# Optimization experiments

Measured on AMD Instinct MI355X. Metric: run time of the kernel, lower is better.

## Reference

```python
import jax, jax.numpy as jnp
import numpy as np

ALPHA = 20.0 / 100.0  # dt / tau


def setup_inputs() -> dict:
    key = jax.random.key(0)
    ks = jax.random.split(key, 5)
    T, B, I, N = 1000, 256, 128, 512
    return {
        "x": jax.random.normal(ks[0], (T, B, I), dtype=jnp.float32),
        "h0": jax.random.normal(ks[1], (B, N), dtype=jnp.float32) * 0.3,
        "W_in": jax.random.normal(ks[2], (N, I), dtype=jnp.float32) / np.sqrt(I),
        "b_in": jax.random.normal(ks[3], (N,), dtype=jnp.float32) * 0.01,
        "W_hh": jax.random.normal(ks[4], (N, N), dtype=jnp.float32) / np.sqrt(N),
    }


def reference(x, h0, W_in, b_in, W_hh):
    # Precompute input projection for all steps in one GEMM: [T,B,N]
    xproj = jnp.einsum("tbi,ni->tbn", x, W_in) + b_in

    def step(h, xp_t):
        h_new = jnp.tanh(xp_t + h @ W_hh.T)
        h = h * (1.0 - ALPHA) + h_new * ALPHA
        return h, h

    hidden, output = jax.lax.scan(step, h0, xproj)
    return output, hidden
```

## Files before the change

### kernel.cpp

```cpp
#include <hip/hip_runtime.h>
#include <hip/hip_bf16.h>


typedef __bf16 bf16;
typedef __bf16 bf16x8 __attribute__((ext_vector_type(8)));
typedef float floatx4 __attribute__((ext_vector_type(4)));
typedef unsigned short u16;
typedef u16 u16x4 __attribute__((ext_vector_type(4)));

#define T_STEPS 1000
#define BATCH 256
#define NDIM 512
#define IDIM 128

__global__ void pack_kernel(const float* __restrict__ W_hh,
                            const float* __restrict__ W_in,
                            bf16x8* __restrict__ Whpack,
                            bf16x8* __restrict__ WinHi,
                            bf16x8* __restrict__ WinLo) {
    int e = blockIdx.x * 256 + threadIdx.x;
    if (e < 32768) {
        int g = e >> 10, s = (e >> 6) & 15, lane = e & 63;
        int n = 16 * g + (lane & 15);
        int k = 32 * s + 8 * (lane >> 4);
        const float* src = W_hh + n * 512 + k;
        bf16x8 v;
#pragma unroll
        for (int j = 0; j < 8; j++) v[j] = (bf16)src[j];
        Whpack[e] = v;
    } else {
        int e2 = e - 32768;
        if (e2 < 8192) {
            int g = e2 >> 8, s = (e2 >> 6) & 3, lane = e2 & 63;
            int n = 16 * g + (lane & 15);
            int i = 32 * s + 8 * (lane >> 4);
            const float* src = W_in + n * 128 + i;
            bf16x8 vh, vl;
#pragma unroll
            for (int j = 0; j < 8; j++) {
                float w = src[j];
                bf16 h = (bf16)w;
                vh[j] = h;
                vl[j] = (bf16)(w - (float)h);
            }
            WinHi[e2] = vh;
            WinLo[e2] = vl;
        }
    }
}

__global__ __launch_bounds__(256)
void xproj_kernel(const float* __restrict__ x,
                  const float* __restrict__ b_in,
                  const bf16x8* __restrict__ WinHi,
                  const bf16x8* __restrict__ WinLo,
                  float* __restrict__ out) {
    int wave = threadIdx.x >> 6, lane = threadIdx.x & 63;
    int m = lane & 15, q = lane >> 4;
    long Mtile = (long)blockIdx.x * 4 + wave;
    long r0 = Mtile * 16;

    bf16x8 ah[4], al[4];
    const float* xrow = x + (r0 + m) * IDIM + q * 8;
#pragma unroll
    for (int s = 0; s < 4; s++) {
#pragma unroll
        for (int j = 0; j < 8; j++) {
            float w = xrow[s * 32 + j];
            bf16 h = (bf16)w;
            ah[s][j] = h;
            al[s][j] = (bf16)(w - (float)h);
        }
    }
    float* orow = out + r0 * NDIM;
#pragma unroll 1
    for (int g = 0; g < 32; g++) {
        floatx4 acc = {0.f, 0.f, 0.f, 0.f};
#pragma unroll
        for (int s = 0; s < 4; s++) {
            bf16x8 bh = WinHi[(g * 4 + s) * 64 + lane];
            bf16x8 bl = WinLo[(g * 4 + s) * 64 + lane];
            acc = __builtin_amdgcn_mfma_f32_16x16x32_bf16(ah[s], bh, acc, 0, 0, 0);
            acc = __builtin_amdgcn_mfma_f32_16x16x32_bf16(al[s], bh, acc, 0, 0, 0);
            acc = __builtin_amdgcn_mfma_f32_16x16x32_bf16(ah[s], bl, acc, 0, 0, 0);
        }
        float b = b_in[16 * g + m];
#pragma unroll
        for (int r = 0; r < 4; r++) {
            orow[(long)(q * 4 + r) * NDIM + 16 * g + m] = acc[r] + b;
        }
    }
}

__global__ __launch_bounds__(512, 2)
void scan_kernel(const float* __restrict__ h0,
                 const bf16x8* __restrict__ Whpack,
                 float* __restrict__ out) {
    extern __shared__ char smem[];
    bf16x8* Wlds = (bf16x8*)smem;
    bf16x8* pack = (bf16x8*)(smem + 128 * 1024);

    const int tid = threadIdx.x;
    const int wave = tid >> 6, lane = tid & 63;
    const int m = lane & 15, q = lane >> 4;
    const int b0 = blockIdx.x * 16;

    bf16x8 Wr[3][16];
    {
        const bf16x8* base = Whpack + (4 * wave) * 1024 + lane;
#pragma unroll
        for (int i = 0; i < 3; i++)
#pragma unroll
            for (int s = 0; s < 16; s++)
                Wr[i][s] = base[(i * 16 + s) * 64];
    }
    for (int r = 0; r < 16; r++) {
        int e = r * 512 + tid;
        int slot = e >> 10;
        int rem = e & 1023;
        Wlds[e] = Whpack[(4 * slot + 3) * 1024 + rem];
    }
    floatx4 h32[4];
#pragma unroll
    for (int i = 0; i < 4; i++) {
        int n0 = (4 * wave + i) * 16 + q * 4;
        h32[i] = *(const floatx4*)(h0 + (b0 + m) * NDIM + n0);
    }
    for (int e = tid; e < 1024; e += 512) {
        int s = e >> 6, l = e & 63;
        const float* src = h0 + (b0 + (l & 15)) * NDIM + s * 32 + 8 * (l >> 4);
        bf16x8 v;
#pragma unroll
        for (int j = 0; j < 8; j++) v[j] = (bf16)src[j];
        pack[e] = v;
    }
    __syncthreads();

    const int wslot = wave * 1024;

#pragma unroll 1
    for (int t = 0; t < T_STEPS; t++) {
        float* row = out + ((long)(t * BATCH + b0 + m)) * NDIM;
        floatx4 xp[4];
#pragma unroll
        for (int i = 0; i < 4; i++) {
            int n0 = (4 * wave + i) * 16 + q * 4;
            xp[i] = *(const floatx4*)(row + n0);
        }

        floatx4 acc[4];
#pragma unroll
        for (int i = 0; i < 4; i++) acc[i] = (floatx4){0.f, 0.f, 0.f, 0.f};

#pragma unroll
        for (int s = 0; s < 16; s++) {
            bf16x8 hfrag = pack[s * 64 + lane];
#pragma unroll
            for (int i = 0; i < 3; i++)
                acc[i] = __builtin_amdgcn_mfma_f32_16x16x32_bf16(Wr[i][s], hfrag, acc[i], 0, 0, 0);
            bf16x8 wl = Wlds[wslot + s * 64 + lane];
            acc[3] = __builtin_amdgcn_mfma_f32_16x16x32_bf16(wl, hfrag, acc[3], 0, 0, 0);
        }
        __syncthreads();

#pragma unroll
        for (int i = 0; i < 4; i++) {
            int n0 = (4 * wave + i) * 16 + q * 4;
            floatx4 z = xp[i] + acc[i];
            floatx4 hn;
#pragma unroll
            for (int r = 0; r < 4; r++) {
                float e = __builtin_amdgcn_exp2f(z[r] * 2.885390081777927f);
                hn[r] = 1.0f - 2.0f * __builtin_amdgcn_rcpf(e + 1.0f);
            }
            h32[i] = h32[i] * 0.8f + hn * 0.2f;
            *(floatx4*)(row + n0) = h32[i];
            int sp = n0 >> 5;
            int o = (n0 >> 3) & 3;
            u16x4 pw;
#pragma unroll
            for (int r = 0; r < 4; r++) {
                bf16 hb = (bf16)h32[i][r];
                pw[r] = __builtin_bit_cast(u16, hb);
            }
            *(u16x4*)(((char*)pack) + (sp * 64 + m + 16 * o) * 16 + (n0 & 7) * 2) = pw;
        }
        __syncthreads();
    }

    float* hid = out + (long)T_STEPS * BATCH * NDIM;
#pragma unroll
    for (int i = 0; i < 4; i++) {
        int n0 = (4 * wave + i) * 16 + q * 4;
        *(floatx4*)(hid + (b0 + m) * NDIM + n0) = h32[i];
    }
}

extern "C" void kernel_launch(void* const* d_in, const int* in_sizes, int n_in,
                              void* d_out, int out_size, void* d_ws, size_t ws_size,
                              hipStream_t stream) {
    const float* x    = (const float*)d_in[0];
    const float* h0   = (const float*)d_in[1];
    const float* W_in = (const float*)d_in[2];
    const float* b_in = (const float*)d_in[3];
    const float* W_hh = (const float*)d_in[4];
    float* out = (float*)d_out;

    bf16x8* Whpack = (bf16x8*)d_ws;
    bf16x8* WinHi  = (bf16x8*)((char*)d_ws + 524288);
    bf16x8* WinLo  = (bf16x8*)((char*)d_ws + 655360);

    hipFuncSetAttribute((const void*)scan_kernel,
                        hipFuncAttributeMaxDynamicSharedMemorySize, 147456);

    pack_kernel<<<160, 256, 0, stream>>>(W_hh, W_in, Whpack, WinHi, WinLo);
    xproj_kernel<<<4000, 256, 0, stream>>>(x, b_in, WinHi, WinLo, out);
    scan_kernel<<<16, 512, 147456, stream>>>(h0, Whpack, out);
}
```

Measured before the change: 4.121 ms.

## Coalesce xproj output via LDS staging and relax scan barriers

The xproj kernel now has each wave handle two 16-row tiles and two column groups at a time. This reuses the W_in fragments across tiles and uses vectorized x loads. Output tiles go through LDS so they leave as coalesced float4 rows instead of strided scalar stores. In the scan loop, __syncthreads is replaced with an LDS-only waitcnt plus s_barrier so the barriers don't wait on global memory. The per-step h output store is moved after the barrier as a nontemporal store. The main risk is the manual barrier being wrong if any global-memory ordering was relied on.

```diff
diff --git a/kernel.cpp b/kernel.cpp
--- a/kernel.cpp
+++ b/kernel.cpp
@@ -55,39 +55,79 @@
                   const bf16x8* __restrict__ WinHi,
                   const bf16x8* __restrict__ WinLo,
                   float* __restrict__ out) {
-    int wave = threadIdx.x >> 6, lane = threadIdx.x & 63;
-    int m = lane & 15, q = lane >> 4;
-    long Mtile = (long)blockIdx.x * 4 + wave;
-    long r0 = Mtile * 16;
-
-    bf16x8 ah[4], al[4];
-    const float* xrow = x + (r0 + m) * IDIM + q * 8;
-#pragma unroll
-    for (int s = 0; s < 4; s++) {
-#pragma unroll
-        for (int j = 0; j < 8; j++) {
-            float w = xrow[s * 32 + j];
-            bf16 h = (bf16)w;
-            ah[s][j] = h;
-            al[s][j] = (bf16)(w - (float)h);
-        }
-    }
-    float* orow = out + r0 * NDIM;
-#pragma unroll 1
-    for (int g = 0; g < 32; g++) {
-        floatx4 acc = {0.f, 0.f, 0.f, 0.f};
+    __shared__ float stg[4][2][16 * 36];
+    const int wave = threadIdx.x >> 6, lane = threadIdx.x & 63;
+    const int m = lane & 15, q = lane >> 4;
+    const long tile0 = ((long)blockIdx.x * 4 + wave) * 2;
+
+    bf16x8 ah[2][4], al[2][4];
+#pragma unroll
+    for (int tt = 0; tt < 2; tt++) {
+        const floatx4* xr = (const floatx4*)(x + ((tile0 + tt) * 16 + m) * IDIM);
 #pragma unroll
         for (int s = 0; s < 4; s++) {
-            bf16x8 bh = WinHi[(g * 4 + s) * 64 + lane];
-            bf16x8 bl = WinLo[(g * 4 + s) * 64 + lane];
-            acc = __builtin_amdgcn_mfma_f32_16x16x32_bf16(ah[s], bh, acc, 0, 0, 0);
-            acc = __builtin_amdgcn_mfma_f32_16x16x32_bf16(al[s], bh, acc, 0, 0, 0);
-            acc = __builtin_amdgcn_mfma_f32_16x16x32_bf16(ah[s], bl, acc, 0, 0, 0);
-        }
-        float b = b_in[16 * g + m];
-#pragma unroll
-        for (int r = 0; r < 4; r++) {
-            orow[(long)(q * 4 + r) * NDIM + 16 * g + m] = acc[r] + b;
+            floatx4 w0 = xr[s * 8 + q * 2];
+            floatx4 w1 = xr[s * 8 + q * 2 + 1];
+#pragma unroll
+            for (int j = 0; j < 4; j++) {
+                float a0 = w0[j], a1 = w1[j];
+                bf16 h0 = (bf16)a0, h1 = (bf16)a1;
+                ah[tt][s][j] = h0;
+                ah[tt][s][j + 4] = h1;
+                al[tt][s][j] = (bf16)(a0 - (float)h0);
+                al[tt][s][j + 4] = (bf16)(a1 - (float)h1);
+            }
+        }
+    }
+
+    const int rrow = lane >> 3;
+    const int rcol = (lane & 7) * 4;
+
+#pragma unroll 2
+    for (int gp = 0; gp < 16; gp++) {
+        floatx4 acc[2][2];
+#pragma unroll
+        for (int tt = 0; tt < 2; tt++)
+#pragma unroll
+            for (int p = 0; p < 2; p++) acc[tt][p] = (floatx4){0.f, 0.f, 0.f, 0.f};
+
+#pragma unroll
+        for (int s = 0; s < 4; s++) {
+            bf16x8 bh0 = WinHi[((2 * gp) * 4 + s) * 64 + lane];
+            bf16x8 bl0 = WinLo[((2 * gp) * 4 + s) * 64 + lane];
+            bf16x8 bh1 = WinHi[((2 * gp + 1) * 4 + s) * 64 + lane];
+            bf16x8 bl1 = WinLo[((2 * gp + 1) * 4 + s) * 64 + lane];
+#pragma unroll
+            for (int tt = 0; tt < 2; tt++) {
+                acc[tt][0] = __builtin_amdgcn_mfma_f32_16x16x32_bf16(ah[tt][s], bh0, acc[tt][0], 0, 0, 0);
+                acc[tt][0] = __builtin_amdgcn_mfma_f32_16x16x32_bf16(al[tt][s], bh0, acc[tt][0], 0, 0, 0);
+                acc[tt][0] = __builtin_amdgcn_mfma_f32_16x16x32_bf16(ah[tt][s], bl0, acc[tt][0], 0, 0, 0);
+                acc[tt][1] = __builtin_amdgcn_mfma_f32_16x16x32_bf16(ah[tt][s], bh1, acc[tt][1], 0, 0, 0);
+                acc[tt][1] = __builtin_amdgcn_mfma_f32_16x16x32_bf16(al[tt][s], bh1, acc[tt][1], 0, 0, 0);
+                acc[tt][1] = __builtin_amdgcn_mfma_f32_16x16x32_bf16(ah[tt][s], bl1, acc[tt][1], 0, 0, 0);
+            }
+        }
+        float b0v = b_in[16 * (2 * gp) + m];
+        float b1v = b_in[16 * (2 * gp + 1) + m];
+#pragma unroll
+        for (int tt = 0; tt < 2; tt++) {
+            float* T = stg[wave][tt];
+#pragma unroll
+            for (int r = 0; r < 4; r++) {
+                T[(q * 4 + r) * 36 + m] = acc[tt][0][r] + b0v;
+                T[(q * 4 + r) * 36 + 16 + m] = acc[tt][1][r] + b1v;
+            }
+        }
+#pragma unroll
+        for (int tt = 0; tt < 2; tt++) {
+            const float* T = stg[wave][tt];
+            long r0 = (tile0 + tt) * 16;
+#pragma unroll
+            for (int k = 0; k < 2; k++) {
+                int row = k * 8 + rrow;
+                floatx4 v = *(const floatx4*)(T + row * 36 + rcol);
+                *(floatx4*)(out + (r0 + row) * NDIM + 32 * gp + rcol) = v;
+            }
         }
     }
 }
@@ -161,7 +201,9 @@
             bf16x8 wl = Wlds[wslot + s * 64 + lane];
             acc[3] = __builtin_amdgcn_mfma_f32_16x16x32_bf16(wl, hfrag, acc[3], 0, 0, 0);
         }
-        __syncthreads();
+        asm volatile("s_waitcnt lgkmcnt(0)" ::: "memory");
+        __builtin_amdgcn_s_barrier();
+        asm volatile("" ::: "memory");
 
 #pragma unroll
         for (int i = 0; i < 4; i++) {
@@ -174,7 +216,6 @@
                 hn[r] = 1.0f - 2.0f * __builtin_amdgcn_rcpf(e + 1.0f);
             }
             h32[i] = h32[i] * 0.8f + hn * 0.2f;
-            *(floatx4*)(row + n0) = h32[i];
             int sp = n0 >> 5;
             int o = (n0 >> 3) & 3;
             u16x4 pw;
@@ -185,7 +226,15 @@
             }
             *(u16x4*)(((char*)pack) + (sp * 64 + m + 16 * o) * 16 + (n0 & 7) * 2) = pw;
         }
-        __syncthreads();
+        asm volatile("s_waitcnt lgkmcnt(0)" ::: "memory");
+        __builtin_amdgcn_s_barrier();
+        asm volatile("" ::: "memory");
+
+#pragma unroll
+        for (int i = 0; i < 4; i++) {
+            int n0 = (4 * wave + i) * 16 + q * 4;
+            __builtin_nontemporal_store(h32[i], (floatx4*)(row + n0));
+        }
     }
 
     float* hid = out + (long)T_STEPS * BATCH * NDIM;
@@ -214,6 +263,6 @@
                         hipFuncAttributeMaxDynamicSharedMemorySize, 147456);
 
     pack_kernel<<<160, 256, 0, stream>>>(W_hh, W_in, Whpack, WinHi, WinLo);
-    xproj_kernel<<<4000, 256, 0, stream>>>(x, b_in, WinHi, WinLo, out);
+    xproj_kernel<<<2000, 256, 0, stream>>>(x, b_in, WinHi, WinLo, out);
     scan_kernel<<<16, 512, 147456, stream>>>(h0, Whpack, out);
 }
```

New measurement: 4.180 ms. About the same (+1.4%).
